# Kernel optimization log

Hardware: AMD Instinct MI355X
Metric: run time of the kernel (lower is better)

Reference implementation:

```python
import jax, jax.numpy as jnp
import numpy as np

B, S, HIDDEN = 2, 2048, 2048
HQ, HKV, D = 16, 4, 128
EPS = 1e-6
SCALE = D ** -0.5


def _deinterleave(x):
    # [..., D] interleaved pairs -> [x0,x2,...,x1,x3,...] (half layout)
    *lead, d = x.shape
    return x.reshape(*lead, d // 2, 2).swapaxes(-1, -2).reshape(*lead, d)


def _interleave(x):
    # inverse of _deinterleave
    *lead, d = x.shape
    return x.reshape(*lead, 2, d // 2).swapaxes(-1, -2).reshape(*lead, d)


def _rotate_half(x):
    x1, x2 = jnp.split(x, 2, axis=-1)
    return jnp.concatenate([-x2, x1], axis=-1)


def _rmsnorm(x, w):
    var = jnp.mean(jnp.square(x), axis=-1, keepdims=True)
    return x * jax.lax.rsqrt(var + EPS) * w


def setup_inputs() -> dict:
    key = jax.random.key(0)
    k0, k1, k2, k3, k4 = jax.random.split(key, 5)
    hidden_states = jax.random.normal(k0, (B, S, HIDDEN), jnp.float32)
    cos = jax.random.uniform(k1, (S, D), jnp.float32, -1.0, 1.0)
    sin = jax.random.uniform(k2, (S, D), jnp.float32, -1.0, 1.0)
    qkv_w = jax.random.normal(k3, ((HQ + 2 * HKV) * D, HIDDEN), jnp.float32) * 0.02
    qk_norm_w = jnp.ones((D,), jnp.float32)
    o_w = jax.random.normal(k4, (HIDDEN, HQ * D), jnp.float32) * 0.02
    return {"hidden_states": hidden_states, "cos": cos, "sin": sin,
            "qkv_w": qkv_w, "qk_norm_w": qk_norm_w, "o_w": o_w}


def reference(hidden_states, cos, sin, qkv_w, qk_norm_w, o_w):
    b, s, _ = hidden_states.shape
    qkv = jnp.einsum('bsh,oh->bso', hidden_states, qkv_w)  # [B,S,(HQ+2HKV)*D]
    q = qkv[..., : HQ * D].reshape(b, s, HQ, D)
    k = qkv[..., HQ * D:(HQ + HKV) * D].reshape(b, s, HKV, D)
    v = qkv[..., (HQ + HKV) * D:].reshape(b, s, HKV, D)

    # interleaved-layout RoPE: deinterleave -> rotate-half RoPE -> re-interleave
    q, k = _deinterleave(q), _deinterleave(k)
    cs = cos[None, :, None, :]
    sn = sin[None, :, None, :]
    q = q * cs + _rotate_half(q) * sn
    k = k * cs + _rotate_half(k) * sn
    q, k = _interleave(q), _interleave(k)

    # QK RMSNorm (shared weight over head_dim)
    q = _rmsnorm(q, qk_norm_w)
    k = _rmsnorm(k, qk_norm_w)

    # causal GQA attention
    g = HQ // HKV
    qg = q.reshape(b, s, HKV, g, D)
    scores = jnp.einsum('bshgd,bthd->bhgst', qg, k) * SCALE  # [B,HKV,g,S,S]
    causal = jnp.tril(jnp.ones((s, s), bool))
    scores = jnp.where(causal, scores, jnp.finfo(scores.dtype).min)
    probs = jax.nn.softmax(scores, axis=-1)
    attn = jnp.einsum('bhgst,bthd->bshgd', probs, v).reshape(b, s, HQ * D)

    return jnp.einsum('bsd,od->bso', attn, o_w)
```

## Files before the change

### kernel.cpp

```cpp
#include <hip/hip_runtime.h>
#include <hip/hip_bf16.h>

typedef __bf16 bf16_t;
typedef bf16_t bf16x8 __attribute__((ext_vector_type(8)));
typedef float f32x4 __attribute__((ext_vector_type(4)));
typedef float f32x16 __attribute__((ext_vector_type(16)));
typedef unsigned short u16;
typedef unsigned int u32;

#define B_    2
#define S_    2048
#define HID   2048
#define NQKV  3072
#define HQ_   16
#define HKV_  4
#define D_    128
#define QSCALE_ 0.12751879526600565f

__device__ __forceinline__ u16 f2b(float f) {
    __hip_bfloat16 h = __float2bfloat16(f);
    return *reinterpret_cast<u16*>(&h);
}
__device__ __forceinline__ float b2f(u32 u) {
    u32 v = u << 16;
    float f;
    __builtin_memcpy(&f, &v, 4);
    return f;
}

__global__ __launch_bounds__(256) void cvt3_f32_bf16(const float* __restrict__ i0, u16* __restrict__ o0, int n0,
                                                     const float* __restrict__ i1, u16* __restrict__ o1, int n1,
                                                     const float* __restrict__ i2, u16* __restrict__ o2, int n2) {
    int i = blockIdx.x * 256 + threadIdx.x;
    const float* src; u16* dst; int idx;
    if (i < n0)           { src = i0; dst = o0; idx = i; }
    else if (i < n0 + n1) { src = i1; dst = o1; idx = i - n0; }
    else if (i < n0 + n1 + n2) { src = i2; dst = o2; idx = i - n0 - n1; }
    else return;
    float4 v = reinterpret_cast<const float4*>(src)[idx];
    ushort4 o;
    o.x = f2b(v.x); o.y = f2b(v.y); o.z = f2b(v.z); o.w = f2b(v.w);
    reinterpret_cast<ushort4*>(dst)[idx] = o;
}

template<bool BF16OUT>
__global__ __launch_bounds__(512, 1) void gemm128x256(const u16* __restrict__ A,
                                                      const u16* __restrict__ Bm,
                                                      void* __restrict__ Cv,
                                                      int M, int N, int K) {
    extern __shared__ __align__(16) char smem[];

    const int tid  = threadIdx.x;
    const int lane = tid & 63;
    const int wid  = tid >> 6;
    const int wr = wid >> 2, wc = wid & 3;
    const int lrow = lane & 15, lgrp = lane >> 4;
    const int swz  = (lrow & 7) << 4;

    const int gx = gridDim.x;
    const int nwg = gx * gridDim.y;
    const int id = blockIdx.x + blockIdx.y * gx;
    const int swid = (id & 7) * (nwg >> 3) + (id >> 3);
    const int m0 = (swid % gx) * 128, n0 = (swid / gx) * 256;

    const int stRow = tid >> 3;
    const int stCol = ((((tid & 7) * 16) ^ ((stRow & 7) << 4)) >> 1);
    const u16* aBase = A  + (size_t)(m0 + stRow) * K + stCol;
    const u16* bBase = Bm + (size_t)(n0 + stRow) * K + stCol;

    auto glds = [&](const u16* g, u16* l) {
        __builtin_amdgcn_global_load_lds(
            (const __attribute__((address_space(1))) void*)g,
            (__attribute__((address_space(3))) void*)l, 16, 0, 0);
    };
    auto stA = [&](int buf, int k0) {
        u16* d = (u16*)(smem + buf * 49152) + tid * 8;
        glds(aBase + k0, d);
        glds(aBase + (size_t)64 * K + k0, d + 512 * 8);
    };
    auto stB = [&](int buf, int h, int k0) {
        u16* d = (u16*)(smem + buf * 49152 + 16384 + h * 16384) + tid * 8;
        const u16* g = bBase + (size_t)(128 * h) * K + k0;
        glds(g, d);
        glds(g + (size_t)64 * K, d + 512 * 8);
    };

    f32x4 acc[4][4] = {};
    const int KT = K >> 6;

    stA(0, 0); stB(0, 0, 0); stB(0, 1, 0);

    for (int t = 0; t < KT; ++t) {
        const int cur = t & 1;
        const int kn  = (t + 1) << 6;
        const bool pf = (t + 1 < KT);
        const char* aT = smem + cur * 49152;
        const char* bT = aT + 16384;

        if (pf) {
            stA(cur ^ 1, kn); stB(cur ^ 1, 0, kn); stB(cur ^ 1, 1, kn);
            asm volatile("s_waitcnt vmcnt(6)" ::: "memory");
        } else {
            asm volatile("s_waitcnt vmcnt(0)" ::: "memory");
        }
        __builtin_amdgcn_s_barrier();

        auto ldA = [&](int mi, int ks) -> bf16x8 {
            int row = wr * 64 + mi * 16 + lrow;
            return *(const bf16x8*)(aT + row * 128 + ((ks * 64 + lgrp * 16) ^ swz));
        };
        auto ldB = [&](int ni, int ks) -> bf16x8 {
            int row = wc * 64 + ni * 16 + lrow;
            return *(const bf16x8*)(bT + row * 128 + ((ks * 64 + lgrp * 16) ^ swz));
        };

        bf16x8 a[4][2], b[2][2], b2[2][2];

        #pragma unroll
        for (int mi = 0; mi < 4; ++mi) { a[mi][0] = ldA(mi, 0); a[mi][1] = ldA(mi, 1); }
        #pragma unroll
        for (int ni = 0; ni < 2; ++ni) { b[ni][0] = ldB(ni, 0); b[ni][1] = ldB(ni, 1); }
        __builtin_amdgcn_s_setprio(1);
        #pragma unroll
        for (int mi = 0; mi < 4; ++mi)
            #pragma unroll
            for (int ni = 0; ni < 2; ++ni) {
                acc[mi][ni] = __builtin_amdgcn_mfma_f32_16x16x32_bf16(a[mi][0], b[ni][0], acc[mi][ni], 0, 0, 0);
                acc[mi][ni] = __builtin_amdgcn_mfma_f32_16x16x32_bf16(a[mi][1], b[ni][1], acc[mi][ni], 0, 0, 0);
            }
        __builtin_amdgcn_s_setprio(0);

        #pragma unroll
        for (int ni = 0; ni < 2; ++ni) { b2[ni][0] = ldB(ni + 2, 0); b2[ni][1] = ldB(ni + 2, 1); }
        __builtin_amdgcn_s_setprio(1);
        #pragma unroll
        for (int mi = 0; mi < 4; ++mi)
            #pragma unroll
            for (int ni = 0; ni < 2; ++ni) {
                acc[mi][ni + 2] = __builtin_amdgcn_mfma_f32_16x16x32_bf16(a[mi][0], b2[ni][0], acc[mi][ni + 2], 0, 0, 0);
                acc[mi][ni + 2] = __builtin_amdgcn_mfma_f32_16x16x32_bf16(a[mi][1], b2[ni][1], acc[mi][ni + 2], 0, 0, 0);
            }
        __builtin_amdgcn_s_setprio(0);
        __builtin_amdgcn_s_barrier();
    }

    #pragma unroll
    for (int mi = 0; mi < 4; ++mi)
        #pragma unroll
        for (int ni = 0; ni < 4; ++ni) {
            int r = m0 + wr * 64 + mi * 16 + lgrp * 4;
            int c = n0 + wc * 64 + ni * 16 + lrow;
            if (BF16OUT) {
                u16* o = (u16*)Cv + (size_t)r * N + c;
                #pragma unroll
                for (int i = 0; i < 4; ++i) o[(size_t)i * N] = f2b(acc[mi][ni][i]);
            } else {
                float* p = (float*)Cv + (size_t)r * N + c;
                #pragma unroll
                for (int i = 0; i < 4; ++i) p[(size_t)i * N] = acc[mi][ni][i];
            }
        }
}

__global__ __launch_bounds__(256) void rope_norm_split(const u16* __restrict__ qkvb,
                                                       const float* __restrict__ cosb,
                                                       const float* __restrict__ sinb,
                                                       const float* __restrict__ nw,
                                                       u16* __restrict__ qb,
                                                       u16* __restrict__ kb,
                                                       u16* __restrict__ vb) {
    const int row  = blockIdx.x;
    const int b    = row >> 11;
    const int s    = row & 2047;
    const int wave = threadIdx.x >> 6;
    const int lane = threadIdx.x & 63;
    const u16* base = qkvb + (size_t)row * NQKV;

    const float c0 = cosb[s * 128 + lane];
    const float c1 = cosb[s * 128 + 64 + lane];
    const float s0 = sinb[s * 128 + lane];
    const float s1 = sinb[s * 128 + 64 + lane];
    const float w0 = nw[2 * lane];
    const float w1 = nw[2 * lane + 1];

    for (int h = wave; h < HQ_ + HKV_; h += 4) {
        u32 xw = *(const u32*)(base + h * 128 + 2 * lane);
        float x0 = b2f(xw & 0xffffu), x1 = b2f(xw >> 16);
        float y0 = x0 * c0 - x1 * s0;
        float y1 = x1 * c1 + x0 * s1;
        float ss = y0 * y0 + y1 * y1;
        #pragma unroll
        for (int off = 32; off; off >>= 1) ss += __shfl_xor(ss, off);
        float r = rsqrtf(ss * (1.0f / 128.0f) + 1e-6f);
        float o0 = y0 * r * w0, o1 = y1 * r * w1;
        if (h < HQ_) {
            u32 pack = (u32)f2b(o0 * QSCALE_) | ((u32)f2b(o1 * QSCALE_) << 16);
            *(u32*)(qb + ((size_t)(b * HQ_ + h) * S_ + s) * D_ + 2 * lane) = pack;
        } else {
            u32 pack = (u32)f2b(o0) | ((u32)f2b(o1) << 16);
            *(u32*)(kb + ((size_t)(b * HKV_ + (h - HQ_)) * S_ + s) * D_ + 2 * lane) = pack;
        }
    }
    {
        int h = wave;
        u32 xw = *(const u32*)(base + (HQ_ + HKV_) * 128 + h * 128 + 2 * lane);
        *(u32*)(vb + ((size_t)(b * HKV_ + h) * S_ + s) * D_ + 2 * lane) = xw;
    }
}

__global__ __launch_bounds__(256) void transpose_v(const u16* __restrict__ vb,
                                                   u16* __restrict__ vtb) {
    __shared__ u16 t[64][72];
    const int s0 = blockIdx.x * 64, d0 = blockIdx.y * 64, bh = blockIdx.z;
    const u16* src = vb  + (size_t)bh * S_ * D_;
    u16*       dst = vtb + (size_t)bh * D_ * S_;
    const int tid = threadIdx.x;

    {
        int r = tid >> 3, c8 = (tid & 7) * 8;
        #pragma unroll
        for (int p = 0; p < 2; p++) {
            int rr = r + p * 32;
            *(uint4*)&t[rr][c8] = *(const uint4*)(src + (size_t)(s0 + rr) * D_ + d0 + c8);
        }
    }
    __syncthreads();
    {
        int dd = tid & 63;
        int sb = (tid >> 6) * 8;
        #pragma unroll
        for (int p = 0; p < 2; p++) {
            int ss8 = sb + p * 32;
            union { u16 u[8]; uint4 v; } pk;
            #pragma unroll
            for (int j = 0; j < 8; j++) pk.u[j] = t[ss8 + j][dd];
            *(uint4*)(dst + (size_t)(d0 + dd) * S_ + s0 + ss8) = pk.v;
        }
    }
}

__global__ __launch_bounds__(256, 2) void attn_fwd3(const u16* __restrict__ qb,
                                                    const u16* __restrict__ kb,
                                                    const u16* __restrict__ vtb,
                                                    u16* __restrict__ attn) {
    __shared__ __align__(16) u16 Ks[2][64 * 128];
    __shared__ __align__(16) u16 Vs[2][128 * 64];

    const int bh  = blockIdx.y;
    const int qt  = (bh < 16) ? (15 - (int)blockIdx.x) : (int)blockIdx.x;
    const int b   = bh >> 4, hq = bh & 15, hkv = hq >> 2;
    const int tid = threadIdx.x;
    const int wave = tid >> 6, lane = tid & 63;
    const int l31 = lane & 31, hi = lane >> 5;
    const int swz = (l31 & 7) << 4;

    const u16* Q  = qb  + (size_t)(b * HQ_  + hq ) * S_ * D_;
    const u16* Kp = kb  + (size_t)(b * HKV_ + hkv) * S_ * D_;
    const u16* Vt = vtb + (size_t)(b * HKV_ + hkv) * D_ * S_;
    const int q0w = qt * 128 + wave * 32;
    const int qg  = q0w + l31;

    int kSrc[4], vSrc[4], cLds[4];
    #pragma unroll
    for (int p = 0; p < 4; p++) {
        int c = tid + p * 256;
        int kr = c >> 4, kc = ((c & 15) * 16) ^ ((kr & 7) << 4);
        kSrc[p] = kr * D_ + (kc >> 1);
        int vr = c >> 3, vc = ((c & 7) * 16) ^ ((vr & 7) << 4);
        vSrc[p] = vr * S_ + (vc >> 1);
        cLds[p] = c * 16;
    }

    auto STAGE = [&](int buf, int kv0s) {
        const u16* kbase = Kp + (size_t)kv0s * D_;
        const u16* vbase = Vt + kv0s;
        #pragma unroll
        for (int p = 0; p < 4; p++)
            __builtin_amdgcn_global_load_lds(
                (const __attribute__((address_space(1))) void*)(kbase + kSrc[p]),
                (__attribute__((address_space(3))) void*)((char*)Ks[buf] + cLds[p]), 16, 0, 0);
        #pragma unroll
        for (int p = 0; p < 4; p++)
            __builtin_amdgcn_global_load_lds(
                (const __attribute__((address_space(1))) void*)(vbase + vSrc[p]),
                (__attribute__((address_space(3))) void*)((char*)Vs[buf] + cLds[p]), 16, 0, 0);
    };

    bf16x8 qf[8];
    #pragma unroll
    for (int ds = 0; ds < 8; ds++)
        qf[ds] = *(const bf16x8*)(Q + (size_t)qg * D_ + ds * 16 + hi * 8);

    float m_run = -1e30f, l_run = 0.f;
    f32x16 oacc[4] = {};

    const int nkt = 2 * qt + 2;
    STAGE(0, 0);

    for (int kt = 0; kt < nkt; kt++) {
        const int cur = kt & 1;
        const int kv0 = kt * 64;
        if (kt + 1 < nkt) {
            STAGE(cur ^ 1, kv0 + 64);
            asm volatile("s_waitcnt vmcnt(8)" ::: "memory");
        } else {
            asm volatile("s_waitcnt vmcnt(0)" ::: "memory");
        }
        __builtin_amdgcn_s_barrier();

        const char* ksb = (const char*)Ks[cur];
        const char* vsb = (const char*)Vs[cur];
        const char* rb0 = ksb + l31 * 256;
        const char* rb1 = rb0 + 32 * 256;
        bf16x8 kA[8], kB[8];
        #pragma unroll
        for (int ds = 0; ds < 8; ds++) kA[ds] = *(const bf16x8*)(rb0 + ((ds * 32 + hi * 16) ^ swz));
        #pragma unroll
        for (int ds = 0; ds < 8; ds++) kB[ds] = *(const bf16x8*)(rb1 + ((ds * 32 + hi * 16) ^ swz));

        f32x16 s0a = {}, s0b = {}, s1a = {}, s1b = {};
        __builtin_amdgcn_s_setprio(1);
        #pragma unroll
        for (int ds = 0; ds < 4; ds++) {
            s0a = __builtin_amdgcn_mfma_f32_32x32x16_bf16(kA[ds],     qf[ds],     s0a, 0, 0, 0);
            s0b = __builtin_amdgcn_mfma_f32_32x32x16_bf16(kA[ds + 4], qf[ds + 4], s0b, 0, 0, 0);
            s1a = __builtin_amdgcn_mfma_f32_32x32x16_bf16(kB[ds],     qf[ds],     s1a, 0, 0, 0);
            s1b = __builtin_amdgcn_mfma_f32_32x32x16_bf16(kB[ds + 4], qf[ds + 4], s1b, 0, 0, 0);
        }
        __builtin_amdgcn_s_setprio(0);
        f32x16 sc[2];
        sc[0] = s0a + s0b;
        sc[1] = s1a + s1b;

        bf16x8 vf[4][4];
        #pragma unroll
        for (int ks = 0; ks < 4; ks++)
            #pragma unroll
            for (int d4 = 0; d4 < 4; d4++)
                vf[ks][d4] = *(const bf16x8*)(vsb + (d4 * 32 + l31) * 128
                                                  + ((ks * 32 + hi * 16) ^ swz));
        __builtin_amdgcn_s_barrier();

        if (kv0 + 63 > q0w) {
            #pragma unroll
            for (int blk = 0; blk < 2; blk++)
                #pragma unroll
                for (int r = 0; r < 16; r++) {
                    int kvg = kv0 + blk * 32 + (r & 3) + 8 * (r >> 2) + 4 * hi;
                    if (kvg > qg) sc[blk][r] = -1e30f;
                }
        }

        float t16[16];
        #pragma unroll
        for (int r = 0; r < 16; r++) t16[r] = fmaxf(sc[0][r], sc[1][r]);
        #pragma unroll
        for (int r = 0; r < 8; r++) t16[r] = fmaxf(t16[r], t16[r + 8]);
        #pragma unroll
        for (int r = 0; r < 4; r++) t16[r] = fmaxf(t16[r], t16[r + 4]);
        float mt = fmaxf(fmaxf(t16[0], t16[1]), fmaxf(t16[2], t16[3]));
        mt = fmaxf(mt, __shfl_xor(mt, 32));

        bool noDefer = !__all(mt <= m_run + 8.0f);
        float mnew = m_run;
        if (noDefer) {
            mnew = fmaxf(m_run, mt);
            float alpha = __builtin_amdgcn_exp2f(m_run - mnew);
            l_run *= alpha;
            #pragma unroll
            for (int d4 = 0; d4 < 4; d4++)
                #pragma unroll
                for (int r = 0; r < 16; r++) oacc[d4][r] *= alpha;
            m_run = mnew;
        }

        float la = 0.f;
        u32 pk0[8], pk1[8];
        #pragma unroll
        for (int g = 0; g < 4; g++)
            #pragma unroll
            for (int e = 0; e < 2; e++) {
                float a0 = __builtin_amdgcn_exp2f(sc[0][g * 4 + 2 * e]     - mnew);
                float b0 = __builtin_amdgcn_exp2f(sc[0][g * 4 + 2 * e + 1] - mnew);
                float a1 = __builtin_amdgcn_exp2f(sc[1][g * 4 + 2 * e]     - mnew);
                float b1 = __builtin_amdgcn_exp2f(sc[1][g * 4 + 2 * e + 1] - mnew);
                la += (a0 + b0) + (a1 + b1);
                pk0[g * 2 + e] = (u32)f2b(a0) | ((u32)f2b(b0) << 16);
                pk1[g * 2 + e] = (u32)f2b(a1) | ((u32)f2b(b1) << 16);
            }
        la += __shfl_xor(la, 32);
        l_run += la;

        u32 qk0[8], qk1[8];
        #pragma unroll
        for (int i = 0; i < 8; i++) {
            qk0[i] = __shfl_xor(pk0[i], 32);
            qk1[i] = __shfl_xor(pk1[i], 32);
        }

        #pragma unroll
        for (int ks = 0; ks < 4; ks++) {
            const int i0 = (ks & 1) * 4;
            union { u32 w[4]; bf16x8 v; } pfv;
            if (ks & 2) {
                pfv.w[0] = hi ? qk1[i0 + 2] : pk1[i0 + 0];
                pfv.w[1] = hi ? qk1[i0 + 3] : pk1[i0 + 1];
                pfv.w[2] = hi ? pk1[i0 + 2] : qk1[i0 + 0];
                pfv.w[3] = hi ? pk1[i0 + 3] : qk1[i0 + 1];
            } else {
                pfv.w[0] = hi ? qk0[i0 + 2] : pk0[i0 + 0];
                pfv.w[1] = hi ? qk0[i0 + 3] : pk0[i0 + 1];
                pfv.w[2] = hi ? pk0[i0 + 2] : qk0[i0 + 0];
                pfv.w[3] = hi ? pk0[i0 + 3] : qk0[i0 + 1];
            }
            __builtin_amdgcn_s_setprio(1);
            #pragma unroll
            for (int d4 = 0; d4 < 4; d4++)
                oacc[d4] = __builtin_amdgcn_mfma_f32_32x32x16_bf16(vf[ks][d4], pfv.v, oacc[d4], 0, 0, 0);
            __builtin_amdgcn_s_setprio(0);
        }
    }

    const float inv = 1.0f / l_run;
    u16* sl = (u16*)Ks + wave * (32 * 128);
    #pragma unroll
    for (int d4 = 0; d4 < 4; d4++)
        #pragma unroll
        for (int rp = 0; rp < 8; rp++) {
            int dbyte = d4 * 64 + 16 * (rp >> 1) + 8 * hi + 4 * (rp & 1);
            u32 w = (u32)f2b(oacc[d4][rp * 2] * inv)
                  | ((u32)f2b(oacc[d4][rp * 2 + 1] * inv) << 16);
            *(u32*)((char*)sl + l31 * 256 + (dbyte ^ swz)) = w;
        }
    #pragma unroll
    for (int j = 0; j < 8; j++) {
        int c = lane + j * 64;
        int qL = c >> 4, dc = c & 15;
        uint4 v = *(uint4*)((char*)sl + qL * 256 + ((dc * 16) ^ ((qL & 7) << 4)));
        int qrow = qt * 128 + wave * 32 + qL;
        *(uint4*)(attn + (size_t)(b * S_ + qrow) * (HQ_ * D_) + hq * D_ + dc * 8) = v;
    }
}

extern "C" void kernel_launch(void* const* d_in, const int* in_sizes, int n_in,
                              void* d_out, int out_size, void* d_ws, size_t ws_size,
                              hipStream_t stream) {
    const float* hidden = (const float*)d_in[0];
    const float* cosb   = (const float*)d_in[1];
    const float* sinb   = (const float*)d_in[2];
    const float* qkvw   = (const float*)d_in[3];
    const float* nw     = (const float*)d_in[4];
    const float* ow     = (const float*)d_in[5];
    float* out = (float*)d_out;

    const size_t M  = (size_t)B_ * S_;
    char* ws = (char*)d_ws;
    size_t off = 0;
    u16*   hb    = (u16*)(ws + off); off += M * HID * 2;
    u16*   wqkvb = (u16*)(ws + off); off += (size_t)NQKV * HID * 2;
    u16*   wob   = (u16*)(ws + off); off += (size_t)HID * (HQ_ * D_) * 2;
    u16*   qkvb  = (u16*)(ws + off); off += M * NQKV * 2;
    u16*   qb2   = (u16*)(ws + off); off += (size_t)B_ * HQ_  * S_ * D_ * 2;
    u16*   kb2   = (u16*)(ws + off); off += (size_t)B_ * HKV_ * S_ * D_ * 2;
    u16*   vb2   = (u16*)(ws + off); off += (size_t)B_ * HKV_ * S_ * D_ * 2;
    u16*   vtb   = (u16*)(ws + off); off += (size_t)B_ * HKV_ * S_ * D_ * 2;
    u16*   attn  = hb;

    {
        int n0 = (int)(M * HID / 4);
        int n1 = NQKV * HID / 4;
        int n2 = HID * (HQ_ * D_) / 4;
        int nt = n0 + n1 + n2;
        cvt3_f32_bf16<<<(nt + 255) / 256, 256, 0, stream>>>(hidden, hb, n0,
                                                            qkvw, wqkvb, n1,
                                                            ow, wob, n2);
    }

    const int smemSz = 98304;
    auto* g1 = gemm128x256<true>;
    auto* g2 = gemm128x256<false>;
    hipFuncSetAttribute(reinterpret_cast<const void*>(g1),
                        hipFuncAttributeMaxDynamicSharedMemorySize, smemSz);
    hipFuncSetAttribute(reinterpret_cast<const void*>(g2),
                        hipFuncAttributeMaxDynamicSharedMemorySize, smemSz);

    gemm128x256<true><<<dim3(M / 128, NQKV / 256), 512, smemSz, stream>>>(
        hb, wqkvb, qkvb, (int)M, NQKV, HID);

    rope_norm_split<<<(int)M, 256, 0, stream>>>(qkvb, cosb, sinb, nw, qb2, kb2, vb2);

    transpose_v<<<dim3(S_ / 64, D_ / 64, B_ * HKV_), 256, 0, stream>>>(vb2, vtb);

    attn_fwd3<<<dim3(16, B_ * HQ_), 256, 0, stream>>>(qb2, kb2, vtb, attn);

    gemm128x256<false><<<dim3(M / 128, HID / 256), 512, smemSz, stream>>>(
        attn, wob, out, (int)M, HID, HQ_ * D_);
}
```

Baseline: 219.1 us.

## Enlarge GEMM tiles to 256x256 and switch to 32x32x16 MFMA

Both projection GEMMs now use 256x256 output tiles per workgroup instead of 128x256, with 128 KB of double-buffered LDS. The inner loop uses 32x32x16 bf16 MFMA instructions in place of 16x16x32, cutting LDS fragment reads per flop and raising operand reuse. The cost is half as many workgroups: QKV has 16x12=192 and the output projection has 16x8=128 on a 256-CU part. That leaves some CUs idle and weakens latency hiding. The epilogue's strided scalar stores also change to the 32x32 accumulator layout.

```diff
diff --git a/kernel.cpp b/kernel.cpp
--- a/kernel.cpp
+++ b/kernel.cpp
@@ -44,120 +44,99 @@
 }
 
 template<bool BF16OUT>
-__global__ __launch_bounds__(512, 1) void gemm128x256(const u16* __restrict__ A,
-                                                      const u16* __restrict__ Bm,
-                                                      void* __restrict__ Cv,
-                                                      int M, int N, int K) {
+__global__ __launch_bounds__(512, 1) void gemm256sq(const u16* __restrict__ A,
+                                                    const u16* __restrict__ Bm,
+                                                    void* __restrict__ Cv,
+                                                    int M, int N, int K) {
     extern __shared__ __align__(16) char smem[];
 
     const int tid  = threadIdx.x;
     const int lane = tid & 63;
     const int wid  = tid >> 6;
     const int wr = wid >> 2, wc = wid & 3;
-    const int lrow = lane & 15, lgrp = lane >> 4;
-    const int swz  = (lrow & 7) << 4;
+    const int l31 = lane & 31, hi = lane >> 5;
+    const int swz = (l31 & 7) << 4;
 
     const int gx = gridDim.x;
     const int nwg = gx * gridDim.y;
     const int id = blockIdx.x + blockIdx.y * gx;
     const int swid = (id & 7) * (nwg >> 3) + (id >> 3);
-    const int m0 = (swid % gx) * 128, n0 = (swid / gx) * 256;
+    const int m0 = (swid % gx) * 256, n0 = (swid / gx) * 256;
 
     const int stRow = tid >> 3;
-    const int stCol = ((((tid & 7) * 16) ^ ((stRow & 7) << 4)) >> 1);
-    const u16* aBase = A  + (size_t)(m0 + stRow) * K + stCol;
-    const u16* bBase = Bm + (size_t)(n0 + stRow) * K + stCol;
+    const int stColE = ((((tid & 7) * 16) ^ ((stRow & 7) << 4)) >> 1);
+    const u16* aBase = A  + (size_t)(m0 + stRow) * K + stColE;
+    const u16* bBase = Bm + (size_t)(n0 + stRow) * K + stColE;
 
     auto glds = [&](const u16* g, u16* l) {
         __builtin_amdgcn_global_load_lds(
             (const __attribute__((address_space(1))) void*)g,
             (__attribute__((address_space(3))) void*)l, 16, 0, 0);
     };
-    auto stA = [&](int buf, int k0) {
-        u16* d = (u16*)(smem + buf * 49152) + tid * 8;
-        glds(aBase + k0, d);
-        glds(aBase + (size_t)64 * K + k0, d + 512 * 8);
+    auto stage = [&](int buf, int k0) {
+        u16* ad = (u16*)(smem + buf * 65536) + tid * 8;
+        u16* bd = ad + 16384;
+        #pragma unroll
+        for (int p = 0; p < 4; ++p)
+            glds(aBase + (size_t)(p * 64) * K + k0, ad + p * 4096);
+        #pragma unroll
+        for (int p = 0; p < 4; ++p)
+            glds(bBase + (size_t)(p * 64) * K + k0, bd + p * 4096);
     };
-    auto stB = [&](int buf, int h, int k0) {
-        u16* d = (u16*)(smem + buf * 49152 + 16384 + h * 16384) + tid * 8;
-        const u16* g = bBase + (size_t)(128 * h) * K + k0;
-        glds(g, d);
-        glds(g + (size_t)64 * K, d + 512 * 8);
-    };
-
-    f32x4 acc[4][4] = {};
+
+    f32x16 acc[4][2] = {};
     const int KT = K >> 6;
 
-    stA(0, 0); stB(0, 0, 0); stB(0, 1, 0);
+    stage(0, 0);
 
     for (int t = 0; t < KT; ++t) {
         const int cur = t & 1;
-        const int kn  = (t + 1) << 6;
         const bool pf = (t + 1 < KT);
-        const char* aT = smem + cur * 49152;
-        const char* bT = aT + 16384;
-
         if (pf) {
-            stA(cur ^ 1, kn); stB(cur ^ 1, 0, kn); stB(cur ^ 1, 1, kn);
-            asm volatile("s_waitcnt vmcnt(6)" ::: "memory");
+            stage(cur ^ 1, (t + 1) << 6);
+            asm volatile("s_waitcnt vmcnt(8)" ::: "memory");
         } else {
             asm volatile("s_waitcnt vmcnt(0)" ::: "memory");
         }
         __builtin_amdgcn_s_barrier();
 
-        auto ldA = [&](int mi, int ks) -> bf16x8 {
-            int row = wr * 64 + mi * 16 + lrow;
-            return *(const bf16x8*)(aT + row * 128 + ((ks * 64 + lgrp * 16) ^ swz));
-        };
-        auto ldB = [&](int ni, int ks) -> bf16x8 {
-            int row = wc * 64 + ni * 16 + lrow;
-            return *(const bf16x8*)(bT + row * 128 + ((ks * 64 + lgrp * 16) ^ swz));
-        };
-
-        bf16x8 a[4][2], b[2][2], b2[2][2];
-
-        #pragma unroll
-        for (int mi = 0; mi < 4; ++mi) { a[mi][0] = ldA(mi, 0); a[mi][1] = ldA(mi, 1); }
-        #pragma unroll
-        for (int ni = 0; ni < 2; ++ni) { b[ni][0] = ldB(ni, 0); b[ni][1] = ldB(ni, 1); }
-        __builtin_amdgcn_s_setprio(1);
-        #pragma unroll
-        for (int mi = 0; mi < 4; ++mi)
-            #pragma unroll
-            for (int ni = 0; ni < 2; ++ni) {
-                acc[mi][ni] = __builtin_amdgcn_mfma_f32_16x16x32_bf16(a[mi][0], b[ni][0], acc[mi][ni], 0, 0, 0);
-                acc[mi][ni] = __builtin_amdgcn_mfma_f32_16x16x32_bf16(a[mi][1], b[ni][1], acc[mi][ni], 0, 0, 0);
-            }
-        __builtin_amdgcn_s_setprio(0);
-
-        #pragma unroll
-        for (int ni = 0; ni < 2; ++ni) { b2[ni][0] = ldB(ni + 2, 0); b2[ni][1] = ldB(ni + 2, 1); }
-        __builtin_amdgcn_s_setprio(1);
-        #pragma unroll
-        for (int mi = 0; mi < 4; ++mi)
-            #pragma unroll
-            for (int ni = 0; ni < 2; ++ni) {
-                acc[mi][ni + 2] = __builtin_amdgcn_mfma_f32_16x16x32_bf16(a[mi][0], b2[ni][0], acc[mi][ni + 2], 0, 0, 0);
-                acc[mi][ni + 2] = __builtin_amdgcn_mfma_f32_16x16x32_bf16(a[mi][1], b2[ni][1], acc[mi][ni + 2], 0, 0, 0);
-            }
-        __builtin_amdgcn_s_setprio(0);
+        const char* aT = smem + cur * 65536;
+        const char* bT = aT + 32768;
+
+        #pragma unroll
+        for (int ks = 0; ks < 4; ++ks) {
+            const int kb = (ks * 32 + hi * 16) ^ swz;
+            bf16x8 af[4], bfv[2];
+            #pragma unroll
+            for (int mb = 0; mb < 4; ++mb)
+                af[mb] = *(const bf16x8*)(aT + (wr * 128 + mb * 32 + l31) * 128 + kb);
+            #pragma unroll
+            for (int nb = 0; nb < 2; ++nb)
+                bfv[nb] = *(const bf16x8*)(bT + (wc * 64 + nb * 32 + l31) * 128 + kb);
+            __builtin_amdgcn_s_setprio(1);
+            #pragma unroll
+            for (int mb = 0; mb < 4; ++mb)
+                #pragma unroll
+                for (int nb = 0; nb < 2; ++nb)
+                    acc[mb][nb] = __builtin_amdgcn_mfma_f32_32x32x16_bf16(
+                        af[mb], bfv[nb], acc[mb][nb], 0, 0, 0);
+            __builtin_amdgcn_s_setprio(0);
+        }
         __builtin_amdgcn_s_barrier();
     }
 
     #pragma unroll
-    for (int mi = 0; mi < 4; ++mi)
-        #pragma unroll
-        for (int ni = 0; ni < 4; ++ni) {
-            int r = m0 + wr * 64 + mi * 16 + lgrp * 4;
-            int c = n0 + wc * 64 + ni * 16 + lrow;
-            if (BF16OUT) {
-                u16* o = (u16*)Cv + (size_t)r * N + c;
-                #pragma unroll
-                for (int i = 0; i < 4; ++i) o[(size_t)i * N] = f2b(acc[mi][ni][i]);
-            } else {
-                float* p = (float*)Cv + (size_t)r * N + c;
-                #pragma unroll
-                for (int i = 0; i < 4; ++i) p[(size_t)i * N] = acc[mi][ni][i];
+    for (int mb = 0; mb < 4; ++mb)
+        #pragma unroll
+        for (int nb = 0; nb < 2; ++nb) {
+            const int n = n0 + wc * 64 + nb * 32 + l31;
+            #pragma unroll
+            for (int r = 0; r < 16; ++r) {
+                int m = m0 + wr * 128 + mb * 32 + (r & 3) + 8 * (r >> 2) + 4 * hi;
+                if (BF16OUT)
+                    ((u16*)Cv)[(size_t)m * N + n] = f2b(acc[mb][nb][r]);
+                else
+                    ((float*)Cv)[(size_t)m * N + n] = acc[mb][nb][r];
             }
         }
 }
@@ -476,15 +455,15 @@
                                                             ow, wob, n2);
     }
 
-    const int smemSz = 98304;
-    auto* g1 = gemm128x256<true>;
-    auto* g2 = gemm128x256<false>;
+    const int smemSz = 131072;
+    auto* g1 = gemm256sq<true>;
+    auto* g2 = gemm256sq<false>;
     hipFuncSetAttribute(reinterpret_cast<const void*>(g1),
                         hipFuncAttributeMaxDynamicSharedMemorySize, smemSz);
     hipFuncSetAttribute(reinterpret_cast<const void*>(g2),
                         hipFuncAttributeMaxDynamicSharedMemorySize, smemSz);
 
-    gemm128x256<true><<<dim3(M / 128, NQKV / 256), 512, smemSz, stream>>>(
+    gemm256sq<true><<<dim3(M / 256, NQKV / 256), 512, smemSz, stream>>>(
         hb, wqkvb, qkvb, (int)M, NQKV, HID);
 
     rope_norm_split<<<(int)M, 256, 0, stream>>>(qkvb, cosb, sinb, nw, qb2, kb2, vb2);
@@ -493,6 +472,6 @@
 
     attn_fwd3<<<dim3(16, B_ * HQ_), 256, 0, stream>>>(qb2, kb2, vtb, attn);
 
-    gemm128x256<false><<<dim3(M / 128, HID / 256), 512, smemSz, stream>>>(
+    gemm256sq<false><<<dim3(M / 256, HID / 256), 512, smemSz, stream>>>(
         attn, wob, out, (int)M, HID, HQ_ * D_);
 }
```

Result: slower. 232.8 us (+6.3%).
